# Performance work log

Hardware: AMD Instinct MI355X
Metric: run time of the kernel (lower is better)

The kernel has to match this reference:

```python
import jax, jax.numpy as jnp
import numpy as np

E, K, D, F = 8, 2, 1024, 4096   # num_experts, top_k, d_model, d_ff
EPS = 1e-6


def setup_inputs() -> dict:
    key = jax.random.key(0)
    ks = jax.random.split(key, 5)
    s = 0.02
    return {
        "x": jax.random.normal(ks[0], (2, 2048, D), jnp.float32),
        "gate_w": jax.random.normal(ks[1], (E, D), jnp.float32) * s,   # nn.Linear(d_model, E, bias=False)
        "ln_w": jnp.ones((E, D), jnp.float32),                          # per-expert RMSNorm weight
        "w1": jax.random.normal(ks[2], (E, F, D), jnp.float32) * s,    # per-expert w_1 (torch [out,in])
        "w3": jax.random.normal(ks[3], (E, F, D), jnp.float32) * s,    # per-expert w_3 (gate proj)
        "w2": jax.random.normal(ks[4], (E, D, F), jnp.float32) * s,    # per-expert w_2
    }


def reference(x, gate_w, ln_w, w1, w3, w2):
    orig_shape = x.shape
    xt = x.reshape(-1, orig_shape[-1])                    # [T, D]
    T = xt.shape[0]

    # --- gating: top-k over expert scores, softmax over selected logits ---
    scores = xt @ gate_w.T                                # [T, E]
    top_w, top_i = jax.lax.top_k(scores, K)               # [T, K]
    top_w = jax.nn.softmax(top_w, axis=-1)                # softmax over the top-k only
    # dense combine weights: comb[t, e] = routing weight if expert e selected else 0
    comb = jnp.zeros((T, E), xt.dtype).at[jnp.arange(T)[:, None], top_i].set(top_w)

    # pre-norm input is shared math; RMSNorm scale differs per expert
    inv_rms = jax.lax.rsqrt(jnp.mean(xt * xt, axis=-1, keepdims=True) + EPS)  # [T, 1]

    # --- per-expert gated-SiLU FFN with residual (PositionwiseFeedForward), weighted combine ---
    y = jnp.zeros_like(xt)
    for e in range(E):  # small fixed expert count; each body is a big vectorized GEMM chain
        norm = xt * inv_rms * ln_w[e]                      # [T, D] RMSNorm
        h = jax.nn.silu(norm @ w1[e].T) * (norm @ w3[e].T)  # [T, F] gated activation
        ye = h @ w2[e].T + xt                               # [T, D] residual inside expert FFN
        y = y + comb[:, e:e + 1] * ye
    return y.reshape(orig_shape)
```

## Files before the change

### kernel.cpp

```cpp
#include <hip/hip_runtime.h>
#include <math.h>

#define T_TOK 4096
#define NE    8
#define DM    1024
#define FF    4096
#define MAXS  9216
#define MAX_TILES 72
#define BM 128
#define BN 128
#define BK 64

using bf16x8 = __attribute__((ext_vector_type(8))) __bf16;
using f32x4  = __attribute__((ext_vector_type(4))) float;

__device__ __forceinline__ float bf2f(unsigned short u) {
    union { float f; unsigned int i; } v; v.i = ((unsigned int)u) << 16; return v.f;
}
__device__ __forceinline__ unsigned short f2bf(float f) {
    union { float f; unsigned int u; } v; v.f = f;
    unsigned int u = v.u;
    unsigned int r = (u + 0x7fffu + ((u >> 16) & 1u)) >> 16;
    return (unsigned short)r;
}
__device__ __forceinline__ void load_bf4(const unsigned short* p, float* f) {
    uint2 u = *(const uint2*)p;
    f[0] = bf2f((unsigned short)(u.x & 0xffffu));
    f[1] = bf2f((unsigned short)(u.x >> 16));
    f[2] = bf2f((unsigned short)(u.y & 0xffffu));
    f[3] = bf2f((unsigned short)(u.y >> 16));
}
__device__ __forceinline__ void gl2lds16(unsigned short* lds, const unsigned short* g) {
    __builtin_amdgcn_global_load_lds((__attribute__((address_space(1))) void*)g,
                                     (__attribute__((address_space(3))) void*)lds,
                                     16, 0, 0);
}

__global__ void k_init(int* counts) {
    if (threadIdx.x < NE) counts[threadIdx.x] = 0;
}

__global__ __launch_bounds__(256) void k_cvt(const float* __restrict__ src,
                                             unsigned short* __restrict__ dst, int n4) {
    int i = blockIdx.x * 256 + threadIdx.x;
    if (i >= n4) return;
    float4 v = ((const float4*)src)[i];
    unsigned int o01 = f2bf(v.x) | ((unsigned int)f2bf(v.y) << 16);
    unsigned int o23 = f2bf(v.z) | ((unsigned int)f2bf(v.w) << 16);
    uint2 st; st.x = o01; st.y = o23;
    ((uint2*)dst)[i] = st;
}

__global__ __launch_bounds__(256) void k_gate(
    const float* __restrict__ x, const float* __restrict__ gw,
    float* __restrict__ invr, int* __restrict__ tok_e, float* __restrict__ tok_w,
    int* __restrict__ counts)
{
    int gid  = blockIdx.x * 256 + threadIdx.x;
    int t    = gid >> 6;
    int lane = gid & 63;
    const float* xr = x + (size_t)t * DM;
    float ss = 0.f;
    float g[NE];
#pragma unroll
    for (int e = 0; e < NE; ++e) g[e] = 0.f;
#pragma unroll
    for (int c = 0; c < 4; ++c) {
        int d = c * 256 + lane * 4;
        float4 xv = *(const float4*)(xr + d);
        ss += xv.x*xv.x + xv.y*xv.y + xv.z*xv.z + xv.w*xv.w;
#pragma unroll
        for (int e = 0; e < NE; ++e) {
            float4 wv = *(const float4*)(gw + (size_t)e * DM + d);
            g[e] += xv.x*wv.x + xv.y*wv.y + xv.z*wv.z + xv.w*wv.w;
        }
    }
#pragma unroll
    for (int off = 32; off > 0; off >>= 1) {
        ss += __shfl_down(ss, off);
#pragma unroll
        for (int e = 0; e < NE; ++e) g[e] += __shfl_down(g[e], off);
    }
    if (lane == 0) {
        invr[t] = rsqrtf(ss * (1.f / DM) + 1e-6f);
        float s0 = g[0]; int e0 = 0;
#pragma unroll
        for (int e = 1; e < NE; ++e) if (g[e] > s0) { s0 = g[e]; e0 = e; }
        float s1 = -1e30f; int e1 = 0;
#pragma unroll
        for (int e = 0; e < NE; ++e) if (e != e0 && g[e] > s1) { s1 = g[e]; e1 = e; }
        float ex = __expf(s1 - s0);
        float den = 1.f / (1.f + ex);
        tok_e[t*2]   = e0;  tok_e[t*2+1] = e1;
        tok_w[t*2]   = den; tok_w[t*2+1] = ex * den;
        atomicAdd(&counts[e0], 1);
        atomicAdd(&counts[e1], 1);
    }
}

__global__ void k_scan(const int* __restrict__ counts, int* __restrict__ cursor,
                       int* __restrict__ ntp, int* __restrict__ tile_e, int* __restrict__ tile_m0,
                       int* __restrict__ pair_tok, float* __restrict__ pair_w, int* __restrict__ pair_e)
{
    __shared__ int sseg[NE + 1];
    if (threadIdx.x == 0) {
        int acc = 0, nt = 0;
        for (int e = 0; e < NE; ++e) {
            sseg[e] = acc;
            cursor[e] = acc;
            int ct = counts[e];
            int tiles = (ct + BM - 1) / BM;
            for (int t2 = 0; t2 < tiles; ++t2) { tile_e[nt] = e; tile_m0[nt] = acc + t2 * BM; ++nt; }
            acc += tiles * BM;
        }
        sseg[NE] = acc;
        ntp[0] = nt;
        for (int t2 = nt; t2 < MAX_TILES; ++t2) { tile_e[t2] = 0; tile_m0[t2] = 0; }
    }
    __syncthreads();
    for (int i = threadIdx.x; i < MAXS; i += blockDim.x) {
        pair_tok[i] = 0;
        pair_w[i]   = 0.f;
        int e = NE - 1;
        for (int j = 0; j < NE; ++j) if (i < sseg[j + 1]) { e = j; break; }
        pair_e[i] = e;
    }
}

__global__ __launch_bounds__(256) void k_scatter(
    const int* __restrict__ tok_e, const float* __restrict__ tok_w, int* __restrict__ cursor,
    int* __restrict__ pair_tok, float* __restrict__ pair_w, int* __restrict__ tok_slot)
{
    int t = blockIdx.x * 256 + threadIdx.x;
    if (t >= T_TOK) return;
#pragma unroll
    for (int k = 0; k < 2; ++k) {
        int e = tok_e[t*2 + k];
        int pos = atomicAdd(&cursor[e], 1);
        pair_tok[pos] = t;
        pair_w[pos]   = tok_w[t*2 + k];
        tok_slot[t*2 + k] = pos;
    }
}

__global__ __launch_bounds__(256) void k_build_ag(
    const float* __restrict__ x, const float* __restrict__ lnw,
    const float* __restrict__ invr, const int* __restrict__ pair_tok, const int* __restrict__ pair_e,
    unsigned short* __restrict__ Ag)
{
    int slot = blockIdx.x * 4 + (threadIdx.x >> 6);
    int lane = threadIdx.x & 63;
    int tok = pair_tok[slot];
    int e   = pair_e[slot];
    float sc = invr[tok];
    const float* xr = x + (size_t)tok * DM;
    const float* lr = lnw + (size_t)e * DM;
    unsigned short* orow = Ag + (size_t)slot * DM;
#pragma unroll
    for (int c = 0; c < 4; ++c) {
        int d = c * 256 + lane * 4;
        float4 xv = *(const float4*)(xr + d);
        float4 lv = *(const float4*)(lr + d);
        unsigned int o01 = f2bf(xv.x*sc*lv.x) | ((unsigned int)f2bf(xv.y*sc*lv.y) << 16);
        unsigned int o23 = f2bf(xv.z*sc*lv.z) | ((unsigned int)f2bf(xv.w*sc*lv.w) << 16);
        uint2 st; st.x = o01; st.y = o23;
        *(uint2*)(orow + d) = st;
    }
}

__global__ __launch_bounds__(256, 2) void k_gemm1(
    const unsigned short* __restrict__ Ag, const unsigned short* __restrict__ w1,
    const unsigned short* __restrict__ w3, unsigned short* __restrict__ Hb,
    const int* __restrict__ ntp, const int* __restrict__ tile_e, const int* __restrict__ tile_m0)
{
    int tile = blockIdx.x;
    if (tile >= ntp[0]) return;
    int e  = tile_e[tile];
    int m0 = tile_m0[tile];
    int n0 = blockIdx.y * BN;

    __shared__ __align__(16) unsigned short As[BM * BK];
    __shared__ __align__(16) unsigned short B1s[BN * BK];
    __shared__ __align__(16) unsigned short B3s[BN * BK];

    int tid = threadIdx.x;
    int lane = tid & 63, wv = tid >> 6;
    int wm = wv >> 1, wn = wv & 1;

    const unsigned short* Abase  = Ag + (size_t)m0 * DM;
    const unsigned short* B1base = w1 + (size_t)e * FF * DM + (size_t)n0 * DM;
    const unsigned short* B3base = w3 + (size_t)e * FF * DM + (size_t)n0 * DM;

    f32x4 acc1[4][4], acc3[4][4];
#pragma unroll
    for (int i = 0; i < 4; ++i)
#pragma unroll
        for (int j = 0; j < 4; ++j) { acc1[i][j] = (f32x4)(0.f); acc3[i][j] = (f32x4)(0.f); }

    int q  = lane >> 4;
    int rr = lane & 15;

    for (int kk = 0; kk < DM; kk += BK) {
#pragma unroll
        for (int p = 0; p < 4; ++p) {
            int gi = p * 256 + tid;
            int r = gi >> 3, s = gi & 7;
            int sg = s ^ (r & 7);
            size_t src = (size_t)r * DM + kk + sg * 8;
            gl2lds16(&As[gi * 8],  Abase  + src);
            gl2lds16(&B1s[gi * 8], B1base + src);
            gl2lds16(&B3s[gi * 8], B3base + src);
        }
        __syncthreads();
#pragma unroll
        for (int ks = 0; ks < 2; ++ks) {
            int g = ks * 4 + q;
            bf16x8 af[4], b1f[4], b3f[4];
#pragma unroll
            for (int i = 0; i < 4; ++i) {
                int row = wm * 64 + i * 16 + rr;
                af[i] = *(const bf16x8*)&As[row * 64 + ((g ^ (row & 7)) << 3)];
            }
#pragma unroll
            for (int j = 0; j < 4; ++j) {
                int row = wn * 64 + j * 16 + rr;
                int off = row * 64 + ((g ^ (row & 7)) << 3);
                b1f[j] = *(const bf16x8*)&B1s[off];
                b3f[j] = *(const bf16x8*)&B3s[off];
            }
#pragma unroll
            for (int i = 0; i < 4; ++i)
#pragma unroll
                for (int j = 0; j < 4; ++j) {
                    acc1[i][j] = __builtin_amdgcn_mfma_f32_16x16x32_bf16(af[i], b1f[j], acc1[i][j], 0, 0, 0);
                    acc3[i][j] = __builtin_amdgcn_mfma_f32_16x16x32_bf16(af[i], b3f[j], acc3[i][j], 0, 0, 0);
                }
        }
        __syncthreads();
    }

#pragma unroll
    for (int i = 0; i < 4; ++i) {
        int mb = wm * 64 + i * 16 + q * 4;
#pragma unroll
        for (int j = 0; j < 4; ++j) {
            int nc = n0 + wn * 64 + j * 16 + rr;
#pragma unroll
            for (int r = 0; r < 4; ++r) {
                float v1 = acc1[i][j][r];
                float v3 = acc3[i][j][r];
                float hv = (v1 / (1.f + __expf(-v1))) * v3;
                Hb[(size_t)(m0 + mb + r) * FF + nc] = f2bf(hv);
            }
        }
    }
}

__global__ __launch_bounds__(256, 2) void k_gemm2(
    const unsigned short* __restrict__ Hb, const unsigned short* __restrict__ w2,
    unsigned short* __restrict__ Pout, const float* __restrict__ pair_w,
    const int* __restrict__ ntp, const int* __restrict__ tile_e, const int* __restrict__ tile_m0)
{
    int tile = blockIdx.x;
    if (tile >= ntp[0]) return;
    int e  = tile_e[tile];
    int m0 = tile_m0[tile];
    int n0 = blockIdx.y * BN;

    __shared__ __align__(16) unsigned short As[BM * BK];
    __shared__ __align__(16) unsigned short Bs[BN * BK];

    int tid = threadIdx.x;
    int lane = tid & 63, wv = tid >> 6;
    int wm = wv >> 1, wn = wv & 1;

    const unsigned short* Abase = Hb + (size_t)m0 * FF;
    const unsigned short* Bbase = w2 + (size_t)e * DM * FF + (size_t)n0 * FF;

    f32x4 acc[4][4];
#pragma unroll
    for (int i = 0; i < 4; ++i)
#pragma unroll
        for (int j = 0; j < 4; ++j) acc[i][j] = (f32x4)(0.f);

    int q = lane >> 4, rr = lane & 15;

    for (int kk = 0; kk < FF; kk += BK) {
#pragma unroll
        for (int p = 0; p < 4; ++p) {
            int gi = p * 256 + tid;
            int r = gi >> 3, s = gi & 7;
            int sg = s ^ (r & 7);
            size_t src = (size_t)r * FF + kk + sg * 8;
            gl2lds16(&As[gi * 8], Abase + src);
            gl2lds16(&Bs[gi * 8], Bbase + src);
        }
        __syncthreads();
#pragma unroll
        for (int ks = 0; ks < 2; ++ks) {
            int g = ks * 4 + q;
            bf16x8 af[4], bf[4];
#pragma unroll
            for (int i = 0; i < 4; ++i) {
                int row = wm * 64 + i * 16 + rr;
                af[i] = *(const bf16x8*)&As[row * 64 + ((g ^ (row & 7)) << 3)];
            }
#pragma unroll
            for (int j = 0; j < 4; ++j) {
                int row = wn * 64 + j * 16 + rr;
                bf[j] = *(const bf16x8*)&Bs[row * 64 + ((g ^ (row & 7)) << 3)];
            }
#pragma unroll
            for (int i = 0; i < 4; ++i)
#pragma unroll
                for (int j = 0; j < 4; ++j)
                    acc[i][j] = __builtin_amdgcn_mfma_f32_16x16x32_bf16(af[i], bf[j], acc[i][j], 0, 0, 0);
        }
        __syncthreads();
    }

#pragma unroll
    for (int i = 0; i < 4; ++i) {
        int mb = wm * 64 + i * 16 + q * 4;
#pragma unroll
        for (int j = 0; j < 4; ++j) {
            int nc = n0 + wn * 64 + j * 16 + rr;
#pragma unroll
            for (int r = 0; r < 4; ++r) {
                float pw = pair_w[m0 + mb + r];
                Pout[(size_t)(m0 + mb + r) * DM + nc] = f2bf(acc[i][j][r] * pw);
            }
        }
    }
}

__global__ __launch_bounds__(256) void k_combine(
    const float* __restrict__ x, const unsigned short* __restrict__ Pout,
    const int* __restrict__ tok_slot, float* __restrict__ out)
{
    int idx = blockIdx.x * 256 + threadIdx.x;
    int t = idx >> 8;
    int d = (idx & 255) << 2;
    int s0 = tok_slot[t*2], s1 = tok_slot[t*2+1];
    float4 xv = *(const float4*)(x + (size_t)t * DM + d);
    float p0[4], p1[4];
    load_bf4(Pout + (size_t)s0 * DM + d, p0);
    load_bf4(Pout + (size_t)s1 * DM + d, p1);
    float4 o;
    o.x = xv.x + p0[0] + p1[0];
    o.y = xv.y + p0[1] + p1[1];
    o.z = xv.z + p0[2] + p1[2];
    o.w = xv.w + p0[3] + p1[3];
    *(float4*)(out + (size_t)t * DM + d) = o;
}

extern "C" void kernel_launch(void* const* d_in, const int* in_sizes, int n_in,
                              void* d_out, int out_size, void* d_ws, size_t ws_size,
                              hipStream_t stream)
{
    const float* x   = (const float*)d_in[0];
    const float* gw  = (const float*)d_in[1];
    const float* lnw = (const float*)d_in[2];
    const float* w1  = (const float*)d_in[3];
    const float* w3  = (const float*)d_in[4];
    const float* w2  = (const float*)d_in[5];
    float* out = (float*)d_out;

    char* p = (char*)d_ws;
    auto carve = [&](size_t bytes) { char* r = p; p += (bytes + 255) & ~(size_t)255; return r; };
    const size_t WE = (size_t)NE * FF * DM;
    unsigned short* W1b  = (unsigned short*)carve(WE * 2);
    unsigned short* W3b  = (unsigned short*)carve(WE * 2);
    unsigned short* W2b  = (unsigned short*)carve(WE * 2);
    unsigned short* Ag   = (unsigned short*)carve((size_t)MAXS * DM * 2);
    unsigned short* Hb   = (unsigned short*)carve((size_t)MAXS * FF * 2);
    unsigned short* Pout = (unsigned short*)carve((size_t)MAXS * DM * 2);
    float* invr     = (float*)carve((size_t)T_TOK * 4);
    int*   tok_e    = (int*)carve((size_t)T_TOK * 2 * 4);
    float* tok_w    = (float*)carve((size_t)T_TOK * 2 * 4);
    int*   tok_slot = (int*)carve((size_t)T_TOK * 2 * 4);
    int*   pair_tok = (int*)carve((size_t)MAXS * 4);
    float* pair_w   = (float*)carve((size_t)MAXS * 4);
    int*   pair_e   = (int*)carve((size_t)MAXS * 4);
    int*   counts   = (int*)carve(NE * 4);
    int*   cursor   = (int*)carve(NE * 4);
    int*   ntp      = (int*)carve(4);
    int*   tile_e   = (int*)carve(MAX_TILES * 4);
    int*   tile_m0  = (int*)carve(MAX_TILES * 4);

    int n4 = (int)(WE / 4);
    k_init<<<1, 64, 0, stream>>>(counts);
    k_cvt<<<(n4 + 255) / 256, 256, 0, stream>>>(w1, W1b, n4);
    k_cvt<<<(n4 + 255) / 256, 256, 0, stream>>>(w3, W3b, n4);
    k_cvt<<<(n4 + 255) / 256, 256, 0, stream>>>(w2, W2b, n4);
    k_gate<<<T_TOK * 64 / 256, 256, 0, stream>>>(x, gw, invr, tok_e, tok_w, counts);
    k_scan<<<1, 256, 0, stream>>>(counts, cursor, ntp, tile_e, tile_m0, pair_tok, pair_w, pair_e);
    k_scatter<<<(T_TOK + 255) / 256, 256, 0, stream>>>(tok_e, tok_w, cursor, pair_tok, pair_w, tok_slot);
    k_build_ag<<<MAXS / 4, 256, 0, stream>>>(x, lnw, invr, pair_tok, pair_e, Ag);
    k_gemm1<<<dim3(MAX_TILES, FF / BN), 256, 0, stream>>>(Ag, W1b, W3b, Hb, ntp, tile_e, tile_m0);
    k_gemm2<<<dim3(MAX_TILES, DM / BN), 256, 0, stream>>>(Hb, W2b, Pout, pair_w, ntp, tile_e, tile_m0);
    k_combine<<<T_TOK * DM / 4 / 256, 256, 0, stream>>>(x, Pout, tok_slot, out);
}
```

Baseline: 852.3 us.

## Widen gemm1 tile to 256 columns with 512 threads, swap grid axes, fuse weight casts

The gate/up GEMM now uses 128x256 tiles computed by 8 waves, so each staged A tile is reused across twice as many output columns. Both GEMMs put the N tiles on grid x, which makes consecutive blocks share the same token tile. The three weight-conversion launches are merged into one kernel, and the SiLU division becomes a hardware reciprocal. The larger tile raises LDS use to about 80KB per block, which may limit occupancy, and it halves the number of gemm1 blocks.

After: 863.5 us. Within noise of the previous version (+1.3%).

```diff
diff --git a/kernel.cpp b/kernel.cpp
--- a/kernel.cpp
+++ b/kernel.cpp
@@ -8,7 +8,8 @@
 #define MAXS  9216
 #define MAX_TILES 72
 #define BM 128
-#define BN 128
+#define BN1 256
+#define BN2 128
 #define BK 64
 
 using bf16x8 = __attribute__((ext_vector_type(8))) __bf16;
@@ -40,15 +41,21 @@
     if (threadIdx.x < NE) counts[threadIdx.x] = 0;
 }
 
-__global__ __launch_bounds__(256) void k_cvt(const float* __restrict__ src,
-                                             unsigned short* __restrict__ dst, int n4) {
+__global__ __launch_bounds__(256) void k_cvt3(
+    const float* __restrict__ w2, const float* __restrict__ w1, const float* __restrict__ w3,
+    unsigned short* __restrict__ W2b, unsigned short* __restrict__ W1b, unsigned short* __restrict__ W3b,
+    int n4)
+{
     int i = blockIdx.x * 256 + threadIdx.x;
-    if (i >= n4) return;
-    float4 v = ((const float4*)src)[i];
+    const float* src; unsigned short* dst; int j;
+    if (i < n4)            { src = w2; dst = W2b; j = i; }
+    else if (i < 2 * n4)   { src = w1; dst = W1b; j = i - n4; }
+    else                   { src = w3; dst = W3b; j = i - 2 * n4; }
+    float4 v = ((const float4*)src)[j];
     unsigned int o01 = f2bf(v.x) | ((unsigned int)f2bf(v.y) << 16);
     unsigned int o23 = f2bf(v.z) | ((unsigned int)f2bf(v.w) << 16);
     uint2 st; st.x = o01; st.y = o23;
-    ((uint2*)dst)[i] = st;
+    ((uint2*)dst)[j] = st;
 }
 
 __global__ __launch_bounds__(256) void k_gate(
@@ -168,24 +175,24 @@
     }
 }
 
-__global__ __launch_bounds__(256, 2) void k_gemm1(
+__global__ __launch_bounds__(512, 2) void k_gemm1(
     const unsigned short* __restrict__ Ag, const unsigned short* __restrict__ w1,
     const unsigned short* __restrict__ w3, unsigned short* __restrict__ Hb,
     const int* __restrict__ ntp, const int* __restrict__ tile_e, const int* __restrict__ tile_m0)
 {
-    int tile = blockIdx.x;
+    int tile = blockIdx.y;
     if (tile >= ntp[0]) return;
     int e  = tile_e[tile];
     int m0 = tile_m0[tile];
-    int n0 = blockIdx.y * BN;
+    int n0 = blockIdx.x * BN1;
 
     __shared__ __align__(16) unsigned short As[BM * BK];
-    __shared__ __align__(16) unsigned short B1s[BN * BK];
-    __shared__ __align__(16) unsigned short B3s[BN * BK];
+    __shared__ __align__(16) unsigned short B1s[BN1 * BK];
+    __shared__ __align__(16) unsigned short B3s[BN1 * BK];
 
     int tid = threadIdx.x;
     int lane = tid & 63, wv = tid >> 6;
-    int wm = wv >> 1, wn = wv & 1;
+    int wm = wv >> 2, wn = wv & 3;
 
     const unsigned short* Abase  = Ag + (size_t)m0 * DM;
     const unsigned short* B1base = w1 + (size_t)e * FF * DM + (size_t)n0 * DM;
@@ -202,12 +209,18 @@
 
     for (int kk = 0; kk < DM; kk += BK) {
 #pragma unroll
+        for (int p = 0; p < 2; ++p) {
+            int gi = p * 512 + tid;
+            int r = gi >> 3, s = gi & 7;
+            int sg = s ^ (r & 7);
+            gl2lds16(&As[gi * 8], Abase + (size_t)r * DM + kk + sg * 8);
+        }
+#pragma unroll
         for (int p = 0; p < 4; ++p) {
-            int gi = p * 256 + tid;
+            int gi = p * 512 + tid;
             int r = gi >> 3, s = gi & 7;
             int sg = s ^ (r & 7);
             size_t src = (size_t)r * DM + kk + sg * 8;
-            gl2lds16(&As[gi * 8],  Abase  + src);
             gl2lds16(&B1s[gi * 8], B1base + src);
             gl2lds16(&B3s[gi * 8], B3base + src);
         }
@@ -249,7 +262,7 @@
             for (int r = 0; r < 4; ++r) {
                 float v1 = acc1[i][j][r];
                 float v3 = acc3[i][j][r];
-                float hv = (v1 / (1.f + __expf(-v1))) * v3;
+                float hv = v1 * __builtin_amdgcn_rcpf(1.f + __expf(-v1)) * v3;
                 Hb[(size_t)(m0 + mb + r) * FF + nc] = f2bf(hv);
             }
         }
@@ -261,14 +274,14 @@
     unsigned short* __restrict__ Pout, const float* __restrict__ pair_w,
     const int* __restrict__ ntp, const int* __restrict__ tile_e, const int* __restrict__ tile_m0)
 {
-    int tile = blockIdx.x;
+    int tile = blockIdx.y;
     if (tile >= ntp[0]) return;
     int e  = tile_e[tile];
     int m0 = tile_m0[tile];
-    int n0 = blockIdx.y * BN;
+    int n0 = blockIdx.x * BN2;
 
     __shared__ __align__(16) unsigned short As[BM * BK];
-    __shared__ __align__(16) unsigned short Bs[BN * BK];
+    __shared__ __align__(16) unsigned short Bs[BN2 * BK];
 
     int tid = threadIdx.x;
     int lane = tid & 63, wv = tid >> 6;
@@ -390,14 +403,12 @@
 
     int n4 = (int)(WE / 4);
     k_init<<<1, 64, 0, stream>>>(counts);
-    k_cvt<<<(n4 + 255) / 256, 256, 0, stream>>>(w1, W1b, n4);
-    k_cvt<<<(n4 + 255) / 256, 256, 0, stream>>>(w3, W3b, n4);
-    k_cvt<<<(n4 + 255) / 256, 256, 0, stream>>>(w2, W2b, n4);
+    k_cvt3<<<(3 * n4 + 255) / 256, 256, 0, stream>>>(w2, w1, w3, W2b, W1b, W3b, n4);
     k_gate<<<T_TOK * 64 / 256, 256, 0, stream>>>(x, gw, invr, tok_e, tok_w, counts);
     k_scan<<<1, 256, 0, stream>>>(counts, cursor, ntp, tile_e, tile_m0, pair_tok, pair_w, pair_e);
     k_scatter<<<(T_TOK + 255) / 256, 256, 0, stream>>>(tok_e, tok_w, cursor, pair_tok, pair_w, tok_slot);
     k_build_ag<<<MAXS / 4, 256, 0, stream>>>(x, lnw, invr, pair_tok, pair_e, Ag);
-    k_gemm1<<<dim3(MAX_TILES, FF / BN), 256, 0, stream>>>(Ag, W1b, W3b, Hb, ntp, tile_e, tile_m0);
-    k_gemm2<<<dim3(MAX_TILES, DM / BN), 256, 0, stream>>>(Hb, W2b, Pout, pair_w, ntp, tile_e, tile_m0);
+    k_gemm1<<<dim3(FF / BN1, MAX_TILES), 512, 0, stream>>>(Ag, W1b, W3b, Hb, ntp, tile_e, tile_m0);
+    k_gemm2<<<dim3(DM / BN2, MAX_TILES), 256, 0, stream>>>(Hb, W2b, Pout, pair_w, ntp, tile_e, tile_m0);
     k_combine<<<T_TOK * DM / 4 / 256, 256, 0, stream>>>(x, Pout, tok_slot, out);
 }
```
